# Kernel tuning notes

Measured on AMD Instinct MI355X. Metric: run time of the kernel, lower is better.

The kernel has to match this reference:

```python
import jax, jax.numpy as jnp
import numpy as np

D_MODEL = 1024
NUM_HEADS = 16
D_K = D_MODEL // NUM_HEADS


def setup_inputs() -> dict:
    key = jax.random.key(0)
    ks = jax.random.split(key, 9)
    s = 1.0 / np.sqrt(D_MODEL)
    inp = {
        "x": jax.random.normal(ks[0], (4, 2048, D_MODEL), dtype=jnp.float32),
        "W_q": jax.random.uniform(ks[1], (D_MODEL, D_MODEL), jnp.float32, -s, s),
        "b_q": jax.random.uniform(ks[2], (D_MODEL,), jnp.float32, -s, s),
        "W_k": jax.random.uniform(ks[3], (D_MODEL, D_MODEL), jnp.float32, -s, s),
        "b_k": jax.random.uniform(ks[4], (D_MODEL,), jnp.float32, -s, s),
        "W_v": jax.random.uniform(ks[5], (D_MODEL, D_MODEL), jnp.float32, -s, s),
        "b_v": jax.random.uniform(ks[6], (D_MODEL,), jnp.float32, -s, s),
        "W_o": jax.random.uniform(ks[7], (D_MODEL, D_MODEL), jnp.float32, -s, s),
        "b_o": jax.random.uniform(ks[8], (D_MODEL,), jnp.float32, -s, s),
    }
    return inp


def reference(x, W_q, b_q, W_k, b_k, W_v, b_v, W_o, b_o):
    B, S, _ = x.shape
    # Linear layers (torch convention: y = x @ W.T + b), split into heads -> [B, H, S, d_k]
    def proj(W, b):
        y = jnp.einsum("bsd,ed->bse", x, W) + b
        return y.reshape(B, S, NUM_HEADS, D_K).transpose(0, 2, 1, 3)

    Q = proj(W_q, b_q)
    K = proj(W_k, b_k)
    V = proj(W_v, b_v)

    scale = 1.0 / jnp.sqrt(jnp.asarray(D_K, dtype=x.dtype))
    scores = jnp.einsum("bhqd,bhkd->bhqk", Q, K) * scale  # [B, H, S, S]
    attn = jax.nn.softmax(scores, axis=-1)
    out = jnp.einsum("bhqk,bhkd->bhqd", attn, V)  # [B, H, S, d_k]
    out = out.transpose(0, 2, 1, 3).reshape(B, S, D_MODEL)
    return jnp.einsum("bsd,ed->bse", out, W_o) + b_o
```

## Files before the change

kernel.cpp:

```cpp
#include <hip/hip_runtime.h>
#include <hip/hip_bf16.h>
#include <math.h>


constexpr int D = 1024;
constexpr int H = 16;
constexpr int DK = 64;
constexpr int PSTR = 72;

typedef unsigned short u16;
typedef __attribute__((ext_vector_type(8))) short v8s;
typedef __attribute__((ext_vector_type(4))) float v4f;
typedef const __attribute__((address_space(1))) void gvoid;
typedef __attribute__((address_space(3))) void lvoid;

__device__ __forceinline__ u16 rne_bf16(float f) {
  unsigned u = __float_as_uint(f);
  u += 0x7FFFu + ((u >> 16) & 1u);
  return (u16)(u >> 16);
}

__device__ __forceinline__ unsigned pk_bf16(float a, float b) {
  __hip_bfloat162 t = __float22bfloat162_rn(float2{a, b});
  return *reinterpret_cast<unsigned*>(&t);
}

__global__ __launch_bounds__(256) void split_kernel(
    const float* __restrict__ in, u16* __restrict__ hi, u16* __restrict__ lo, int n4)
{
  const int i = blockIdx.x * 256 + threadIdx.x;
  if (i >= n4) return;
  const float4 v = ((const float4*)in)[i];
  const float f[4] = {v.x, v.y, v.z, v.w};
  ushort4 h, l;
  u16 hh[4], ll[4];
#pragma unroll
  for (int j = 0; j < 4; ++j) {
    const unsigned u = __float_as_uint(f[j]);
    hh[j] = (u16)(u >> 16);
    const float hf = __uint_as_float(u & 0xFFFF0000u);
    ll[j] = rne_bf16(f[j] - hf);
  }
  h.x = hh[0]; h.y = hh[1]; h.z = hh[2]; h.w = hh[3];
  l.x = ll[0]; l.y = ll[1]; l.z = ll[2]; l.w = ll[3];
  ((ushort4*)hi)[i] = h;
  ((ushort4*)lo)[i] = l;
}

struct GemmAcc { v4f a[4][4]; };

__device__ __forceinline__ void gemm_body(
    const u16* __restrict__ Ahi, const u16* __restrict__ Alo,
    const u16* __restrict__ Whi, const u16* __restrict__ Wlo,
    int m0, int nrow0, GemmAcc& g,
    u16* sAhi, u16* sAlo, u16* sBhi, u16* sBlo)
{
  const int tid = threadIdx.x;
  const int lane = tid & 63, w = tid >> 6;
  const int wm = (w >> 1) * 64, wn = (w & 1) * 64;
  const int fr = lane & 15, fq = lane >> 4;
  const int srow = tid >> 2;
  const int skel = (tid & 3) * 8;

  for (int k0 = 0; k0 < D; k0 += 32) {
#pragma unroll
    for (int rep = 0; rep < 2; ++rep) {
      const int row = srow + rep * 64;
      const size_t offA = (size_t)(m0 + row) * D + k0 + skel;
      const size_t offB = (size_t)(nrow0 + row) * D + k0 + skel;
      const int ldso = rep * 2048 + tid * 8;
      __builtin_amdgcn_global_load_lds((gvoid*)(Ahi + offA), (lvoid*)(sAhi + ldso), 16, 0, 0);
      __builtin_amdgcn_global_load_lds((gvoid*)(Alo + offA), (lvoid*)(sAlo + ldso), 16, 0, 0);
      __builtin_amdgcn_global_load_lds((gvoid*)(Whi + offB), (lvoid*)(sBhi + ldso), 16, 0, 0);
      __builtin_amdgcn_global_load_lds((gvoid*)(Wlo + offB), (lvoid*)(sBlo + ldso), 16, 0, 0);
    }
    __syncthreads();

    v8s ahi[4], alo[4], bhi[4], blo[4];
#pragma unroll
    for (int t = 0; t < 4; ++t) {
      const int ar = (wm + t * 16 + fr) * 32 + fq * 8;
      const int br = (wn + t * 16 + fr) * 32 + fq * 8;
      ahi[t] = *(const v8s*)&sAhi[ar];
      alo[t] = *(const v8s*)&sAlo[ar];
      bhi[t] = *(const v8s*)&sBhi[br];
      blo[t] = *(const v8s*)&sBlo[br];
    }
#pragma unroll
    for (int mi = 0; mi < 4; ++mi)
#pragma unroll
      for (int ni = 0; ni < 4; ++ni) {
        g.a[mi][ni] = __builtin_amdgcn_mfma_f32_16x16x32_bf16(ahi[mi], bhi[ni], g.a[mi][ni], 0, 0, 0);
        g.a[mi][ni] = __builtin_amdgcn_mfma_f32_16x16x32_bf16(alo[mi], bhi[ni], g.a[mi][ni], 0, 0, 0);
        g.a[mi][ni] = __builtin_amdgcn_mfma_f32_16x16x32_bf16(ahi[mi], blo[ni], g.a[mi][ni], 0, 0, 0);
      }
    __syncthreads();
  }
}

__global__ __launch_bounds__(256) void gemm_qkv_kernel(
    const u16* __restrict__ Ahi, const u16* __restrict__ Alo,
    const u16* __restrict__ Whi, const u16* __restrict__ Wlo,
    const float* __restrict__ bq, const float* __restrict__ bk, const float* __restrict__ bv,
    u16* __restrict__ Qb, u16* __restrict__ Kb, u16* __restrict__ Vtb,
    int S_)
{
  __shared__ u16 sAhi[128 * 32];
  __shared__ u16 sAlo[128 * 32];
  __shared__ u16 sBhi[128 * 32];
  __shared__ u16 sBlo[128 * 32];

  GemmAcc g;
#pragma unroll
  for (int mi = 0; mi < 4; ++mi)
#pragma unroll
    for (int ni = 0; ni < 4; ++ni) g.a[mi][ni] = (v4f){0.f, 0.f, 0.f, 0.f};

  const int m0 = blockIdx.x * 128;
  gemm_body(Ahi, Alo, Whi, Wlo, m0, blockIdx.y * 128, g, sAhi, sAlo, sBhi, sBlo);

  const int wsel = blockIdx.y >> 3;
  const float* bias = (wsel == 0) ? bq : (wsel == 1) ? bk : bv;
  u16* Cb = (wsel == 0) ? Qb : (wsel == 1) ? Kb : Vtb;
  const int n0l = (blockIdx.y & 7) * 128;

  const int tid = threadIdx.x;
  const int lane = tid & 63, w = tid >> 6;
  const int wm = (w >> 1) * 64, wn = (w & 1) * 64;
  const int fr = lane & 15, fq = lane >> 4;

#pragma unroll
  for (int mi = 0; mi < 4; ++mi) {
#pragma unroll
    for (int ni = 0; ni < 4; ++ni) {
      const int n = n0l + wn + ni * 16 + fr;
      const float bvv = bias[n];
      const int h = n >> 6, dk = n & 63;
#pragma unroll
      for (int r = 0; r < 4; ++r) {
        const int m = m0 + wm + mi * 16 + fq * 4 + r;
        const int b = m / S_, s = m - b * S_;
        const float val = g.a[mi][ni][r] + bvv;
        if (wsel < 2)
          Cb[((size_t)(b * H + h) * S_ + s) * DK + dk] = rne_bf16(val);
        else
          Cb[((size_t)(b * H + h) * DK + dk) * S_ + s] = rne_bf16(val);
      }
    }
  }
}

__global__ __launch_bounds__(256) void gemm_out_kernel(
    const u16* __restrict__ Ahi, const u16* __restrict__ Alo,
    const u16* __restrict__ Whi, const u16* __restrict__ Wlo,
    const float* __restrict__ bias, float* __restrict__ C)
{
  __shared__ u16 sAhi[128 * 32];
  __shared__ u16 sAlo[128 * 32];
  __shared__ u16 sBhi[128 * 32];
  __shared__ u16 sBlo[128 * 32];

  GemmAcc g;
#pragma unroll
  for (int mi = 0; mi < 4; ++mi)
#pragma unroll
    for (int ni = 0; ni < 4; ++ni) g.a[mi][ni] = (v4f){0.f, 0.f, 0.f, 0.f};

  const int m0 = blockIdx.x * 128, n0 = blockIdx.y * 128;
  gemm_body(Ahi, Alo, Whi, Wlo, m0, n0, g, sAhi, sAlo, sBhi, sBlo);

  const int tid = threadIdx.x;
  const int lane = tid & 63, w = tid >> 6;
  const int wm = (w >> 1) * 64, wn = (w & 1) * 64;
  const int fr = lane & 15, fq = lane >> 4;

#pragma unroll
  for (int mi = 0; mi < 4; ++mi)
#pragma unroll
    for (int ni = 0; ni < 4; ++ni) {
      const int n = n0 + wn + ni * 16 + fr;
      const float bvv = bias[n];
#pragma unroll
      for (int r = 0; r < 4; ++r) {
        const int m = m0 + wm + mi * 16 + fq * 4 + r;
        C[(size_t)m * D + n] = g.a[mi][ni][r] + bvv;
      }
    }
}

__global__ __launch_bounds__(256) void attn_mfma_kernel(
    const u16* __restrict__ Qb, const u16* __restrict__ Kb, const u16* __restrict__ Vtb,
    u16* __restrict__ Ohi, u16* __restrict__ Olo, int S_)
{
  __shared__ u16 Ks[64 * 64];
  __shared__ u16 Vt[64 * 64];
  __shared__ u16 Pl[4][32 * PSTR];

  const int tid = threadIdx.x;
  const int lane = tid & 63, w = tid >> 6;
  const int fr = lane & 15, fq = lane >> 4;
  const int q0 = blockIdx.x * 128;
  const int h = blockIdx.y, b = blockIdx.z;
  const int wq = w * 32;
  const size_t base = (size_t)(b * H + h) * S_ * DK;

  const int srow = tid >> 3;
  const int scb = (tid & 7) ^ (srow & 7);

  v8s qa[2][2];
#pragma unroll
  for (int ni = 0; ni < 2; ++ni)
#pragma unroll
    for (int ks = 0; ks < 2; ++ks)
      qa[ni][ks] = *(const v8s*)(Qb + base + (size_t)(q0 + wq + ni * 16 + fr) * DK + ks * 32 + fq * 8);

  v4f o[4][2];
  float lsum[2] = {0.f, 0.f};
#pragma unroll
  for (int mi = 0; mi < 4; ++mi)
#pragma unroll
    for (int ni = 0; ni < 2; ++ni) o[mi][ni] = (v4f){0.f, 0.f, 0.f, 0.f};

  for (int j0 = 0; j0 < S_; j0 += 64) {
    __syncthreads();
#pragma unroll
    for (int rep = 0; rep < 2; ++rep) {
      const int row = rep * 32 + srow;
      const int ldso = rep * 2048 + tid * 8;
      __builtin_amdgcn_global_load_lds((gvoid*)(Kb + base + (size_t)(j0 + row) * DK + scb * 8),
                                       (lvoid*)(Ks + ldso), 16, 0, 0);
      __builtin_amdgcn_global_load_lds((gvoid*)(Vtb + base + (size_t)row * S_ + j0 + scb * 8),
                                       (lvoid*)(Vt + ldso), 16, 0, 0);
    }
    __syncthreads();

    v4f s[4][2];
#pragma unroll
    for (int mi = 0; mi < 4; ++mi)
#pragma unroll
      for (int ni = 0; ni < 2; ++ni) s[mi][ni] = (v4f){0.f, 0.f, 0.f, 0.f};
#pragma unroll
    for (int ks = 0; ks < 2; ++ks) {
      v8s kb[4];
#pragma unroll
      for (int mi = 0; mi < 4; ++mi) {
        const int row = mi * 16 + fr;
        kb[mi] = *(const v8s*)&Ks[row * 64 + (((ks * 4 + fq) ^ (row & 7)) * 8)];
      }
#pragma unroll
      for (int mi = 0; mi < 4; ++mi)
#pragma unroll
        for (int ni = 0; ni < 2; ++ni)
          s[mi][ni] = __builtin_amdgcn_mfma_f32_16x16x32_bf16(kb[mi], qa[ni][ks], s[mi][ni], 0, 0, 0);
    }

#pragma unroll
    for (int mi = 0; mi < 4; ++mi)
#pragma unroll
      for (int ni = 0; ni < 2; ++ni) {
        float p[4];
#pragma unroll
        for (int r = 0; r < 4; ++r) p[r] = __expf(s[mi][ni][r] * 0.125f);
        lsum[ni] += (p[0] + p[1]) + (p[2] + p[3]);
        uint2 pk;
        pk.x = pk_bf16(p[0], p[1]);
        pk.y = pk_bf16(p[2], p[3]);
        *(uint2*)&Pl[w][(ni * 16 + fr) * PSTR + mi * 16 + fq * 4] = pk;
      }

#pragma unroll
    for (int ks = 0; ks < 2; ++ks) {
      v8s vb[4], pa[2];
#pragma unroll
      for (int mi = 0; mi < 4; ++mi) {
        const int row = mi * 16 + fr;
        vb[mi] = *(const v8s*)&Vt[row * 64 + (((ks * 4 + fq) ^ (row & 7)) * 8)];
      }
#pragma unroll
      for (int ni = 0; ni < 2; ++ni)
        pa[ni] = *(const v8s*)&Pl[w][(ni * 16 + fr) * PSTR + ks * 32 + fq * 8];
#pragma unroll
      for (int mi = 0; mi < 4; ++mi)
#pragma unroll
        for (int ni = 0; ni < 2; ++ni)
          o[mi][ni] = __builtin_amdgcn_mfma_f32_16x16x32_bf16(vb[mi], pa[ni], o[mi][ni], 0, 0, 0);
    }
  }

  float linv[2];
#pragma unroll
  for (int ni = 0; ni < 2; ++ni) {
    float l = lsum[ni];
    l += __shfl_xor(l, 16);
    l += __shfl_xor(l, 32);
    linv[ni] = 1.f / l;
  }

#pragma unroll
  for (int ni = 0; ni < 2; ++ni) {
    const int q = q0 + wq + ni * 16 + fr;
    const size_t rowbase = (size_t)(b * S_ + q) * D + h * DK;
#pragma unroll
    for (int mi = 0; mi < 4; ++mi) {
      const int d0 = mi * 16 + fq * 4;
      float v[4];
      unsigned u[4];
      float res[4];
#pragma unroll
      for (int r = 0; r < 4; ++r) {
        v[r] = o[mi][ni][r] * linv[ni];
        u[r] = __float_as_uint(v[r]);
        res[r] = v[r] - __uint_as_float(u[r] & 0xFFFF0000u);
      }
      uint2 hi, lo;
      hi.x = (u[1] & 0xFFFF0000u) | (u[0] >> 16);
      hi.y = (u[3] & 0xFFFF0000u) | (u[2] >> 16);
      lo.x = pk_bf16(res[0], res[1]);
      lo.y = pk_bf16(res[2], res[3]);
      *(uint2*)(Ohi + rowbase + d0) = hi;
      *(uint2*)(Olo + rowbase + d0) = lo;
    }
  }
}

extern "C" void kernel_launch(void* const* d_in, const int* in_sizes, int n_in,
                              void* d_out, int out_size, void* d_ws, size_t ws_size,
                              hipStream_t stream) {
  const float* x  = (const float*)d_in[0];
  const float* Wq = (const float*)d_in[1];
  const float* bq = (const float*)d_in[2];
  const float* Wk = (const float*)d_in[3];
  const float* bk = (const float*)d_in[4];
  const float* Wv = (const float*)d_in[5];
  const float* bv = (const float*)d_in[6];
  const float* Wo = (const float*)d_in[7];
  const float* bo = (const float*)d_in[8];

  const int M = in_sizes[0] / D;
  const int B = 4;
  const int S_ = M / B;
  const size_t MD = (size_t)M * D;
  const size_t DD = (size_t)D * D;

  u16* Qb    = (u16*)d_ws;
  u16* Kb    = Qb + MD;
  u16* Vtb   = Kb + MD;
  u16* xs_hi = Vtb + MD;
  u16* xs_lo = xs_hi + MD;
  u16* Ohi   = xs_lo + MD;
  u16* Olo   = Ohi + MD;
  u16* wo_hi = Olo + MD;
  u16* wo_lo = wo_hi + DD;

  u16* wqkv_hi = (u16*)d_out;
  u16* wqkv_lo = wqkv_hi + 3 * DD;

  const int gx = (int)(MD / 4 / 256);
  const int gw = (int)(DD / 4 / 256);

  split_kernel<<<gx, 256, 0, stream>>>(x,  xs_hi, xs_lo, (int)(MD / 4));
  split_kernel<<<gw, 256, 0, stream>>>(Wq, wqkv_hi,          wqkv_lo,          (int)(DD / 4));
  split_kernel<<<gw, 256, 0, stream>>>(Wk, wqkv_hi + DD,     wqkv_lo + DD,     (int)(DD / 4));
  split_kernel<<<gw, 256, 0, stream>>>(Wv, wqkv_hi + 2 * DD, wqkv_lo + 2 * DD, (int)(DD / 4));
  split_kernel<<<gw, 256, 0, stream>>>(Wo, wo_hi, wo_lo, (int)(DD / 4));

  dim3 gq(M / 128, 3 * D / 128);
  gemm_qkv_kernel<<<gq, 256, 0, stream>>>(xs_hi, xs_lo, wqkv_hi, wqkv_lo,
                                          bq, bk, bv, Qb, Kb, Vtb, S_);

  dim3 ga(S_ / 128, H, B);
  attn_mfma_kernel<<<ga, 256, 0, stream>>>(Qb, Kb, Vtb, Ohi, Olo, S_);

  dim3 go(M / 128, D / 128);
  gemm_out_kernel<<<go, 256, 0, stream>>>(Ohi, Olo, wo_hi, wo_lo, bo, (float*)d_out);
}
```

Measured before the change: 432.7 us.

## Replace split-bf16 GEMMs with 8-wave multi-buffered pipelined large-tile kernel

Both projection GEMMs now use one templated kernel with 512 threads and 256x256 (QKV) or 128x256 (output) tiles. The hi/lo split passes become separate k-tiles streamed through a 4-slot LDS ring, prefetched three stages ahead with explicit vmcnt waits. The kernel also adds an XOR swizzle to cut LDS bank conflicts, remaps block IDs across XCDs, and raises wave priority around the MFMA bursts. The goal is to hide global-load latency and improve data reuse, at the cost of large LDS use (about 128KB for the QKV tile), which limits occupancy to one block per CU.

```diff
diff --git a/kernel.cpp b/kernel.cpp
--- a/kernel.cpp
+++ b/kernel.cpp
@@ -47,145 +47,146 @@
   ((ushort4*)lo)[i] = l;
 }
 
-struct GemmAcc { v4f a[4][4]; };
-
-__device__ __forceinline__ void gemm_body(
+template<int R>
+__device__ __forceinline__ void stage_arr(const u16* __restrict__ src, u16* dst,
+                                          int tid, int row0, int k0)
+{
+  const int cg = (tid & 3) ^ ((tid >> 3) & 3);
+#pragma unroll
+  for (int j = 0; j < R / 128; ++j) {
+    const int row = j * 128 + (tid >> 2);
+    __builtin_amdgcn_global_load_lds(
+        (gvoid*)(src + (size_t)(row0 + row) * D + k0 + cg * 8),
+        (lvoid*)(dst + j * 4096 + tid * 8), 16, 0, 0);
+  }
+}
+
+template<int BM, int BN, int EPI>
+__global__ __launch_bounds__(512, 2) void gemm8p_kernel(
     const u16* __restrict__ Ahi, const u16* __restrict__ Alo,
     const u16* __restrict__ Whi, const u16* __restrict__ Wlo,
-    int m0, int nrow0, GemmAcc& g,
-    u16* sAhi, u16* sAlo, u16* sBhi, u16* sBlo)
+    const float* __restrict__ b0, const float* __restrict__ b1, const float* __restrict__ b2,
+    u16* __restrict__ Qb, u16* __restrict__ Kb, u16* __restrict__ Vtb,
+    float* __restrict__ C, int S_)
 {
+  constexpr int LA = BM * 32;
+  constexpr int LB = BN * 32;
+  constexpr int RM = BM / 32;
+  constexpr int RN = BN / 64;
+  __shared__ u16 lds[4][LA + LB];
+
   const int tid = threadIdx.x;
   const int lane = tid & 63, w = tid >> 6;
-  const int wm = (w >> 1) * 64, wn = (w & 1) * 64;
+  const int wm = (w >> 2) * (BM / 2), wn = (w & 3) * (BN / 4);
   const int fr = lane & 15, fq = lane >> 4;
-  const int srow = tid >> 2;
-  const int skel = (tid & 3) * 8;
-
-  for (int k0 = 0; k0 < D; k0 += 32) {
-#pragma unroll
-    for (int rep = 0; rep < 2; ++rep) {
-      const int row = srow + rep * 64;
-      const size_t offA = (size_t)(m0 + row) * D + k0 + skel;
-      const size_t offB = (size_t)(nrow0 + row) * D + k0 + skel;
-      const int ldso = rep * 2048 + tid * 8;
-      __builtin_amdgcn_global_load_lds((gvoid*)(Ahi + offA), (lvoid*)(sAhi + ldso), 16, 0, 0);
-      __builtin_amdgcn_global_load_lds((gvoid*)(Alo + offA), (lvoid*)(sAlo + ldso), 16, 0, 0);
-      __builtin_amdgcn_global_load_lds((gvoid*)(Whi + offB), (lvoid*)(sBhi + ldso), 16, 0, 0);
-      __builtin_amdgcn_global_load_lds((gvoid*)(Wlo + offB), (lvoid*)(sBlo + ldso), 16, 0, 0);
-    }
-    __syncthreads();
-
-    v8s ahi[4], alo[4], bhi[4], blo[4];
-#pragma unroll
-    for (int t = 0; t < 4; ++t) {
-      const int ar = (wm + t * 16 + fr) * 32 + fq * 8;
-      const int br = (wn + t * 16 + fr) * 32 + fq * 8;
-      ahi[t] = *(const v8s*)&sAhi[ar];
-      alo[t] = *(const v8s*)&sAlo[ar];
-      bhi[t] = *(const v8s*)&sBhi[br];
-      blo[t] = *(const v8s*)&sBlo[br];
-    }
-#pragma unroll
-    for (int mi = 0; mi < 4; ++mi)
-#pragma unroll
-      for (int ni = 0; ni < 4; ++ni) {
-        g.a[mi][ni] = __builtin_amdgcn_mfma_f32_16x16x32_bf16(ahi[mi], bhi[ni], g.a[mi][ni], 0, 0, 0);
-        g.a[mi][ni] = __builtin_amdgcn_mfma_f32_16x16x32_bf16(alo[mi], bhi[ni], g.a[mi][ni], 0, 0, 0);
-        g.a[mi][ni] = __builtin_amdgcn_mfma_f32_16x16x32_bf16(ahi[mi], blo[ni], g.a[mi][ni], 0, 0, 0);
-      }
-    __syncthreads();
-  }
-}
-
-__global__ __launch_bounds__(256) void gemm_qkv_kernel(
-    const u16* __restrict__ Ahi, const u16* __restrict__ Alo,
-    const u16* __restrict__ Whi, const u16* __restrict__ Wlo,
-    const float* __restrict__ bq, const float* __restrict__ bk, const float* __restrict__ bv,
-    u16* __restrict__ Qb, u16* __restrict__ Kb, u16* __restrict__ Vtb,
-    int S_)
-{
-  __shared__ u16 sAhi[128 * 32];
-  __shared__ u16 sAlo[128 * 32];
-  __shared__ u16 sBhi[128 * 32];
-  __shared__ u16 sBlo[128 * 32];
-
-  GemmAcc g;
-#pragma unroll
-  for (int mi = 0; mi < 4; ++mi)
-#pragma unroll
-    for (int ni = 0; ni < 4; ++ni) g.a[mi][ni] = (v4f){0.f, 0.f, 0.f, 0.f};
-
-  const int m0 = blockIdx.x * 128;
-  gemm_body(Ahi, Alo, Whi, Wlo, m0, blockIdx.y * 128, g, sAhi, sAlo, sBhi, sBlo);
-
-  const int wsel = blockIdx.y >> 3;
-  const float* bias = (wsel == 0) ? bq : (wsel == 1) ? bk : bv;
-  u16* Cb = (wsel == 0) ? Qb : (wsel == 1) ? Kb : Vtb;
-  const int n0l = (blockIdx.y & 7) * 128;
-
-  const int tid = threadIdx.x;
-  const int lane = tid & 63, w = tid >> 6;
-  const int wm = (w >> 1) * 64, wn = (w & 1) * 64;
-  const int fr = lane & 15, fq = lane >> 4;
-
-#pragma unroll
-  for (int mi = 0; mi < 4; ++mi) {
-#pragma unroll
-    for (int ni = 0; ni < 4; ++ni) {
-      const int n = n0l + wn + ni * 16 + fr;
-      const float bvv = bias[n];
-      const int h = n >> 6, dk = n & 63;
-#pragma unroll
-      for (int r = 0; r < 4; ++r) {
-        const int m = m0 + wm + mi * 16 + fq * 4 + r;
-        const int b = m / S_, s = m - b * S_;
-        const float val = g.a[mi][ni][r] + bvv;
-        if (wsel < 2)
-          Cb[((size_t)(b * H + h) * S_ + s) * DK + dk] = rne_bf16(val);
-        else
-          Cb[((size_t)(b * H + h) * DK + dk) * S_ + s] = rne_bf16(val);
-      }
-    }
-  }
-}
-
-__global__ __launch_bounds__(256) void gemm_out_kernel(
-    const u16* __restrict__ Ahi, const u16* __restrict__ Alo,
-    const u16* __restrict__ Whi, const u16* __restrict__ Wlo,
-    const float* __restrict__ bias, float* __restrict__ C)
-{
-  __shared__ u16 sAhi[128 * 32];
-  __shared__ u16 sAlo[128 * 32];
-  __shared__ u16 sBhi[128 * 32];
-  __shared__ u16 sBlo[128 * 32];
-
-  GemmAcc g;
-#pragma unroll
-  for (int mi = 0; mi < 4; ++mi)
-#pragma unroll
-    for (int ni = 0; ni < 4; ++ni) g.a[mi][ni] = (v4f){0.f, 0.f, 0.f, 0.f};
-
-  const int m0 = blockIdx.x * 128, n0 = blockIdx.y * 128;
-  gemm_body(Ahi, Alo, Whi, Wlo, m0, n0, g, sAhi, sAlo, sBhi, sBlo);
-
-  const int tid = threadIdx.x;
-  const int lane = tid & 63, w = tid >> 6;
-  const int wm = (w >> 1) * 64, wn = (w & 1) * 64;
-  const int fr = lane & 15, fq = lane >> 4;
-
-#pragma unroll
-  for (int mi = 0; mi < 4; ++mi)
-#pragma unroll
-    for (int ni = 0; ni < 4; ++ni) {
-      const int n = n0 + wn + ni * 16 + fr;
-      const float bvv = bias[n];
-#pragma unroll
-      for (int r = 0; r < 4; ++r) {
-        const int m = m0 + wm + mi * 16 + fq * 4 + r;
-        C[(size_t)m * D + n] = g.a[mi][ni][r] + bvv;
-      }
-    }
+  const int csw = (fq ^ ((fr >> 1) & 3)) * 8;
+
+  const int gx = gridDim.x;
+  const int nwg = gx * gridDim.y;
+  int id = blockIdx.y * gx + blockIdx.x;
+  id = (id & 7) * (nwg >> 3) + (id >> 3);
+  const int m0 = (id % gx) * BM;
+  const int n0 = (id / gx) * BN;
+
+  v4f acc[RM][RN];
+#pragma unroll
+  for (int mi = 0; mi < RM; ++mi)
+#pragma unroll
+    for (int ni = 0; ni < RN; ++ni) acc[mi][ni] = (v4f){0.f, 0.f, 0.f, 0.f};
+
+#pragma unroll
+  for (int p = 0; p < 3; ++p) {
+    const u16* As = (p == 1) ? Alo : Ahi;
+    const u16* Bs = (p == 2) ? Wlo : Whi;
+    stage_arr<BM>(As, &lds[p][0], tid, m0, 0);
+    stage_arr<BN>(Bs, &lds[p][LA], tid, n0, 0);
+  }
+
+  for (int pk4 = 0; pk4 < 32; pk4 += 4) {
+#pragma unroll
+    for (int dpk = 0; dpk < 4; ++dpk) {
+#pragma unroll
+      for (int p = 0; p < 3; ++p) {
+        const int ktl = 3 * dpk + p;
+        const int buf = ktl & 3;
+        const int sbuf = (ktl + 3) & 3;
+
+        if constexpr (BM == 256) {
+          asm volatile("s_waitcnt vmcnt(8) lgkmcnt(0)" ::: "memory");
+        } else {
+          asm volatile("s_waitcnt vmcnt(6) lgkmcnt(0)" ::: "memory");
+        }
+        __builtin_amdgcn_s_barrier();
+        asm volatile("" ::: "memory");
+
+        v8s af[RM], bfr[RN];
+#pragma unroll
+        for (int mi = 0; mi < RM; ++mi)
+          af[mi] = *(const v8s*)&lds[buf][(wm + mi * 16 + fr) * 32 + csw];
+#pragma unroll
+        for (int ni = 0; ni < RN; ++ni)
+          bfr[ni] = *(const v8s*)&lds[buf][LA + (wn + ni * 16 + fr) * 32 + csw];
+
+        {
+          const int pk = pk4 + dpk;
+          const int pks = (pk + 1 < 32) ? pk + 1 : 31;
+          const u16* As = (p == 1) ? Alo : Ahi;
+          const u16* Bs = (p == 2) ? Wlo : Whi;
+          stage_arr<BM>(As, &lds[sbuf][0], tid, m0, pks * 32);
+          stage_arr<BN>(Bs, &lds[sbuf][LA], tid, n0, pks * 32);
+        }
+
+        __builtin_amdgcn_s_setprio(1);
+#pragma unroll
+        for (int mi = 0; mi < RM; ++mi)
+#pragma unroll
+          for (int ni = 0; ni < RN; ++ni)
+            acc[mi][ni] = __builtin_amdgcn_mfma_f32_16x16x32_bf16(af[mi], bfr[ni], acc[mi][ni], 0, 0, 0);
+        __builtin_amdgcn_s_setprio(0);
+      }
+    }
+  }
+
+  const int lane4 = fq * 4;
+  if constexpr (EPI == 0) {
+    const int wsel = n0 >> 10;
+    const float* bias = (wsel == 0) ? b0 : (wsel == 1) ? b1 : b2;
+    u16* Cb = (wsel == 0) ? Qb : (wsel == 1) ? Kb : Vtb;
+    const int bb = m0 / S_;
+    const int s0 = m0 - bb * S_;
+#pragma unroll
+    for (int mi = 0; mi < RM; ++mi) {
+#pragma unroll
+      for (int ni = 0; ni < RN; ++ni) {
+        const int n = n0 + wn + ni * 16 + fr;
+        const int nl = n & (D - 1);
+        const float bvv = bias[nl];
+        const int h = nl >> 6, dk = nl & 63;
+#pragma unroll
+        for (int r = 0; r < 4; ++r) {
+          const int s = s0 + wm + mi * 16 + lane4 + r;
+          const float val = acc[mi][ni][r] + bvv;
+          if (wsel < 2)
+            Cb[((size_t)(bb * H + h) * S_ + s) * DK + dk] = rne_bf16(val);
+          else
+            Cb[((size_t)(bb * H + h) * DK + dk) * S_ + s] = rne_bf16(val);
+        }
+      }
+    }
+  } else {
+#pragma unroll
+    for (int mi = 0; mi < RM; ++mi)
+#pragma unroll
+      for (int ni = 0; ni < RN; ++ni) {
+        const int n = n0 + wn + ni * 16 + fr;
+        const float bvv = b0[n];
+#pragma unroll
+        for (int r = 0; r < 4; ++r) {
+          const int m = m0 + wm + mi * 16 + lane4 + r;
+          C[(size_t)m * D + n] = acc[mi][ni][r] + bvv;
+        }
+      }
+  }
 }
 
 __global__ __launch_bounds__(256) void attn_mfma_kernel(
@@ -364,13 +365,15 @@
   split_kernel<<<gw, 256, 0, stream>>>(Wv, wqkv_hi + 2 * DD, wqkv_lo + 2 * DD, (int)(DD / 4));
   split_kernel<<<gw, 256, 0, stream>>>(Wo, wo_hi, wo_lo, (int)(DD / 4));
 
-  dim3 gq(M / 128, 3 * D / 128);
-  gemm_qkv_kernel<<<gq, 256, 0, stream>>>(xs_hi, xs_lo, wqkv_hi, wqkv_lo,
-                                          bq, bk, bv, Qb, Kb, Vtb, S_);
+  dim3 gq(M / 256, 3 * D / 256);
+  gemm8p_kernel<256, 256, 0><<<gq, 512, 0, stream>>>(
+      xs_hi, xs_lo, wqkv_hi, wqkv_lo, bq, bk, bv, Qb, Kb, Vtb, nullptr, S_);
 
   dim3 ga(S_ / 128, H, B);
   attn_mfma_kernel<<<ga, 256, 0, stream>>>(Qb, Kb, Vtb, Ohi, Olo, S_);
 
-  dim3 go(M / 128, D / 128);
-  gemm_out_kernel<<<go, 256, 0, stream>>>(Ohi, Olo, wo_hi, wo_lo, bo, (float*)d_out);
-}
+  dim3 go(M / 128, D / 256);
+  gemm8p_kernel<128, 256, 1><<<go, 512, 0, stream>>>(
+      Ohi, Olo, wo_hi, wo_lo, bo, nullptr, nullptr, nullptr, nullptr, nullptr,
+      (float*)d_out, S_);
+}
```

Result: slower. 507.2 us (+17.2%).
